# Kernel optimization log

Hardware: AMD Instinct MI355X
Metric: run time of the kernel (lower is better)

## Reference

```python
import jax, jax.numpy as jnp
import numpy as np

P_LEN, Q_LEN, BATCH, D, H = 300, 50, 32, 256, 256


def _make_params(key):
    ks = jax.random.split(key, 6)
    s = lambda k, shape, fan: jax.random.normal(k, shape, jnp.float32) * (1.0 / np.sqrt(fan))
    return dict(
        Wq=s(ks[0], (2, H, D), D), bq=jnp.zeros((2, H), jnp.float32),
        Wp=s(ks[1], (2, H, D), D), bp=jnp.zeros((2, H), jnp.float32),
        Wr=s(ks[2], (2, H, H), H), br=jnp.zeros((2, H), jnp.float32),
        Wg=s(ks[3], (2, H), H), bg=jnp.zeros((2,), jnp.float32),
        ln_g=jnp.ones((2, 2 * D), jnp.float32), ln_b=jnp.zeros((2, 2 * D), jnp.float32),
        W_ih=s(ks[4], (2, 4 * H, 2 * D), 2 * D), W_hh=s(ks[5], (2, 4 * H, H), H),
        b_ih=jnp.zeros((2, 4 * H), jnp.float32), b_hh=jnp.zeros((2, 4 * H), jnp.float32),
    )


def setup_inputs() -> dict:
    key = jax.random.key(0)
    k1, k2, k3, k4, kp = jax.random.split(key, 5)
    content_vec = jax.random.normal(k1, (P_LEN, BATCH, D), jnp.float32)
    question_vec = jax.random.normal(k2, (Q_LEN, BATCH, D), jnp.float32)
    p_len = jax.random.randint(k3, (BATCH,), P_LEN // 2, P_LEN + 1)
    q_len = jax.random.randint(k4, (BATCH,), Q_LEN // 2, Q_LEN + 1)
    content_mask = (jnp.arange(P_LEN)[None, :] < p_len[:, None]).astype(jnp.int32)
    question_mask = (jnp.arange(Q_LEN)[None, :] < q_len[:, None]).astype(jnp.int32)
    inp = dict(content_vec=content_vec, content_mask=content_mask,
               question_vec=question_vec, question_mask=question_mask)
    inp.update(_make_params(kp))
    return inp


def _masked_flip(v, mask):
    # v: (P, B, D); mask: (B, P). Reverses the valid prefix of each sequence,
    # leaving padding positions in place (standard Match-LSTM masked_flip).
    P = v.shape[0]
    lengths = mask.sum(axis=1)  # (B,)
    t = jnp.arange(P)[:, None]  # (P, 1)
    idx = jnp.where(t < lengths[None, :], lengths[None, :] - 1 - t, t)  # (P, B)
    idx = jnp.broadcast_to(idx[:, :, None], v.shape)
    return jnp.take_along_axis(v, idx, axis=0)


def _uni_match(cv, qv, qmask, Wq, bq, Wp, bp, Wr, br, Wg, bg, ln_g, ln_b, W_ih, W_hh, b_ih, b_hh):
    # cv: (P, B, D), qv: (Q, B, D), qmask: (B, Q)
    B = cv.shape[1]
    Hh = Wr.shape[0]
    wh = jnp.einsum('qbd,hd->qbh', qv, Wq) + bq      # (Q, B, H), precomputed once
    hp_all = jnp.einsum('pbd,hd->pbh', cv, Wp) + bp  # (P, B, H), precomputed
    pad = (qmask == 0)                               # (B, Q)

    def step(carry, xs):
        h, c = carry
        cv_t, hp_t = xs
        hr = h @ Wr.T + br                                    # (B, H)
        g = jnp.tanh(wh + hp_t[None] + hr[None])              # (Q, B, H)
        alpha = (jnp.einsum('qbh,h->qb', g, Wg) + bg).T       # (B, Q)
        alpha = jax.nn.softmax(jnp.where(pad, -jnp.inf, alpha), axis=1)
        h_alpha = jnp.einsum('bq,qbd->bd', alpha, qv)         # (B, D)
        z = jnp.concatenate([cv_t, h_alpha], axis=1)          # (B, 2D)
        mu = jnp.mean(z, axis=-1, keepdims=True)
        var = jnp.mean((z - mu) ** 2, axis=-1, keepdims=True)
        z = (z - mu) * jax.lax.rsqrt(var + 1e-5) * ln_g + ln_b
        gates = z @ W_ih.T + b_ih + h @ W_hh.T + b_hh         # (B, 4H)
        i_, f_, g_, o_ = jnp.split(gates, 4, axis=1)          # torch LSTMCell order i,f,g,o
        c_n = jax.nn.sigmoid(f_) * c + jax.nn.sigmoid(i_) * jnp.tanh(g_)
        h_n = jax.nn.sigmoid(o_) * jnp.tanh(c_n)
        return (h_n, c_n), h_n

    h0 = jnp.zeros((B, Hh), cv.dtype)
    _, hs = jax.lax.scan(step, (h0, h0), (cv, hp_all))
    return hs  # (P, B, H)


def reference(content_vec, content_mask, question_vec, question_mask,
              Wq, bq, Wp, bp, Wr, br, Wg, bg, ln_g, ln_b, W_ih, W_hh, b_ih, b_hh):
    # Dropout with p=0 (inference) is identity.
    args = lambda i: (Wq[i], bq[i], Wp[i], bp[i], Wr[i], br[i], Wg[i], bg[i],
                      ln_g[i], ln_b[i], W_ih[i], W_hh[i], b_ih[i], b_hh[i])
    right = _uni_match(content_vec, question_vec, question_mask, *args(0))
    cv_flip = _masked_flip(content_vec, content_mask)
    left = _uni_match(cv_flip, question_vec, question_mask, *args(1))
    left = _masked_flip(left, content_mask)
    res = jnp.concatenate([right, left], axis=2)            # (P, B, 2H)
    return content_mask.T[:, :, None].astype(res.dtype) * res
```

## Files before the change

kernel.cpp:

```cpp
#include <hip/hip_runtime.h>
#include <hip/hip_fp16.h>

typedef unsigned int u32;
typedef unsigned long long u64;
typedef _Float16 half2_t __attribute__((ext_vector_type(2)));
typedef _Float16 f16x8 __attribute__((ext_vector_type(8)));
typedef float f32x16 __attribute__((ext_vector_type(16)));

static constexpr int PL = 300;
static constexpr int QL = 50;
static constexpr int B  = 32;
static constexpr int D  = 256;
static constexpr int H  = 256;

__device__ __forceinline__ float fdot2(u32 w, u32 x, float acc) {
    return __builtin_amdgcn_fdot2(__builtin_bit_cast(half2_t, w),
                                  __builtin_bit_cast(half2_t, x), acc, false);
}
__device__ __forceinline__ u32 packh2(float a, float b) {
    half2_t h2; h2[0] = (_Float16)a; h2[1] = (_Float16)b;
    return __builtin_bit_cast(u32, h2);
}
__device__ __forceinline__ f32x16 mfma16(uint4 a, uint4 b, f32x16 c) {
    return __builtin_amdgcn_mfma_f32_32x32x16_f16(
        __builtin_bit_cast(f16x8, a), __builtin_bit_cast(f16x8, b), c, 0, 0, 0);
}
__device__ __forceinline__ u32 a_ld32(const u32* p) {
    return __hip_atomic_load(p, __ATOMIC_RELAXED, __HIP_MEMORY_SCOPE_AGENT);
}
__device__ __forceinline__ u64 a_ld64(const u64* p) {
    return __hip_atomic_load(p, __ATOMIC_RELAXED, __HIP_MEMORY_SCOPE_AGENT);
}
__device__ __forceinline__ void a_st32(u32* p, u32 v) {
    __hip_atomic_store(p, v, __ATOMIC_RELAXED, __HIP_MEMORY_SCOPE_AGENT);
}
__device__ __forceinline__ void a_st64(u64* p, u64 v) {
    __hip_atomic_store(p, v, __ATOMIC_RELAXED, __HIP_MEMORY_SCOPE_AGENT);
}

__global__ __launch_bounds__(256) void pack_wt2(const float* __restrict__ Whh,
                                                const float* __restrict__ Wr,
                                                u32* __restrict__ dst) {
    int id = blockIdx.x * 256 + threadIdx.x;
    int u  = id & 127;
    int rw = (id >> 7) % 40;
    int j  = ((id >> 7) / 40) % 32;
    int dd = (id >> 7) / 1280;
    float a, c;
    if (rw < 32) {
        int R = (rw >> 3) * 256 + 8 * j + (rw & 7);
        a = Whh[((size_t)dd * 1024 + R) * 256 + 2 * u];
        c = Whh[((size_t)dd * 1024 + R) * 256 + 2 * u + 1];
    } else {
        int wrr = 8 * j + (rw - 32);
        a = Wr[((size_t)dd * 256 + wrr) * 256 + 2 * u];
        c = Wr[((size_t)dd * 256 + wrr) * 256 + 2 * u + 1];
    }
    dst[id] = packh2(a, c);
}

__global__ __launch_bounds__(256) void prep_proj(const float* __restrict__ X,
                                                 const float* __restrict__ W,
                                                 const float* __restrict__ Bv,
                                                 __half* __restrict__ out,
                                                 int T, int nt) {
    int id = blockIdx.x;
    int tb = id % nt; id /= nt;
    int b  = id % B;  id /= B;
    int g  = id;
    int t0 = tb * 8;
    int nr = T - t0; if (nr > 8) nr = 8;
    __shared__ __align__(16) float xs[8][256];
    int tid = threadIdx.x;
    for (int r = 0; r < nr; r++) xs[r][tid] = X[((t0 + r) * B + b) * D + tid];
    __syncthreads();
    const float4* wrow = (const float4*)&W[(g * H + tid) * D];
    float bb = Bv[g * H + tid];
    float acc[8];
#pragma unroll
    for (int r = 0; r < 8; r++) acc[r] = bb;
    for (int d4 = 0; d4 < D / 4; d4++) {
        float4 w = wrow[d4];
#pragma unroll
        for (int r = 0; r < 8; r++) {
            float4 x = *(const float4*)&xs[r][d4 * 4];
            acc[r] = fmaf(w.x, x.x, fmaf(w.y, x.y, fmaf(w.z, x.z, fmaf(w.w, x.w, acc[r]))));
        }
    }
    for (int r = 0; r < nr; r++)
        out[((g * B + b) * T + t0 + r) * H + tid] = __float2half(acc[r]);
}

__global__ __launch_bounds__(256) void p1_prep(const float* __restrict__ cv,
                                               const float* __restrict__ Wih,
                                               const float* __restrict__ lng,
                                               __half* __restrict__ P1) {
    int id = blockIdx.x;
    int tb = id % 38; id /= 38;
    int b  = id % 32; id /= 32;
    int dd = id;
    int t0 = tb * 8;
    int nr = PL - t0; if (nr > 8) nr = 8;
    __shared__ __align__(16) float xs[8][256];
    int tid = threadIdx.x;
    float g = lng[dd * 512 + tid];
    for (int r = 0; r < nr; r++)
        xs[r][tid] = cv[((size_t)(t0 + r) * B + b) * D + tid] * g;
    __syncthreads();
    for (int gc = 0; gc < 4; gc++) {
        int R = gc * 256 + tid;
        const float4* wrow = (const float4*)&Wih[((size_t)dd * 1024 + R) * 512];
        float acc[8] = {};
        for (int d4 = 0; d4 < 64; d4++) {
            float4 w = wrow[d4];
#pragma unroll
            for (int r = 0; r < 8; r++) {
                float4 x = *(const float4*)&xs[r][d4 * 4];
                acc[r] = fmaf(w.x, x.x, fmaf(w.y, x.y, fmaf(w.z, x.z, fmaf(w.w, x.w, acc[r]))));
            }
        }
        for (int r = 0; r < nr; r++)
            P1[((size_t)(dd * 32 + b) * PL + t0 + r) * 1024 + R] = __float2half(acc[r]);
    }
}

__global__ __launch_bounds__(256) void vp_prep(const float* __restrict__ qv,
                                               const float* __restrict__ Wih,
                                               const float* __restrict__ lng,
                                               __half* __restrict__ VP) {
    int blk = blockIdx.x;
    int dd = blk >> 8, b = (blk >> 3) & 31, rc = blk & 7;
    __shared__ __align__(16) u32 qg[50 * 128];
    __shared__ __align__(16) u32 wch[128 * 128];
    int tid = threadIdx.x;
    for (int v = tid; v < 6400; v += 256) {
        int q = v >> 7, i = v & 127;
        float a = qv[((size_t)q * 32 + b) * 256 + 2 * i]     * lng[dd * 512 + 256 + 2 * i];
        float c = qv[((size_t)q * 32 + b) * 256 + 2 * i + 1] * lng[dd * 512 + 256 + 2 * i + 1];
        qg[v] = packh2(a, c);
    }
    for (int v = tid; v < 16384; v += 256) {
        int rl = v >> 7, i = v & 127;
        int r = rc * 128 + rl;
        float a = Wih[((size_t)dd * 1024 + r) * 512 + 256 + 2 * i];
        float c = Wih[((size_t)dd * 1024 + r) * 512 + 256 + 2 * i + 1];
        wch[v] = packh2(a, c);
    }
    __syncthreads();
    for (int p = tid; p < 128 * 56; p += 256) {
        int rl = p / 56, q = p % 56;
        int r = rc * 128 + rl;
        float acc = 0.f;
        if (q < 50) {
            const u32* qr = qg + q * 128;
            const u32* wr = wch + rl * 128;
#pragma unroll 8
            for (int i = 0; i < 128; i++) acc = fdot2(wr[i], qr[i], acc);
        }
        VP[((size_t)(dd * 32 + b) * 1024 + r) * 56 + q] = __float2half(acc);
    }
}

__global__ __launch_bounds__(256) void gram_prep(const float* __restrict__ qv,
                                                 float* __restrict__ G,
                                                 float* __restrict__ qs) {
    int b = blockIdx.x;
    __shared__ float qvs[50 * 256];
    int tid = threadIdx.x;
    for (int v = tid; v < 12800; v += 256) {
        int q = v >> 8, k = v & 255;
        qvs[v] = qv[((size_t)q * 32 + b) * 256 + k];
    }
    __syncthreads();
    for (int p = tid; p < 2500; p += 256) {
        int q = p / 50, q2 = p % 50;
        float acc = 0.f;
        for (int k = 0; k < 256; k++) acc = fmaf(qvs[q * 256 + k], qvs[q2 * 256 + k], acc);
        G[((size_t)b * 50 + q) * 50 + q2] = acc;
    }
    if (tid < 52) {
        float s = 0.f;
        if (tid < 50) for (int k = 0; k < 256; k++) s += qvs[tid * 256 + k];
        qs[b * 52 + tid] = s;
    }
}

__global__ __launch_bounds__(256) void cvstats_prep(const float* __restrict__ cv,
                                                    float* __restrict__ st) {
    int blk = blockIdx.x;
    int t = blk >> 5, b = blk & 31;
    int tid = threadIdx.x;
    float v = cv[((size_t)t * 32 + b) * 256 + tid];
    float s = v, s2 = v * v;
#pragma unroll
    for (int m = 32; m; m >>= 1) { s += __shfl_xor(s, m, 64); s2 += __shfl_xor(s2, m, 64); }
    __shared__ float red[8];
    if ((tid & 63) == 0) { red[(tid >> 6) * 2] = s; red[(tid >> 6) * 2 + 1] = s2; }
    __syncthreads();
    if (tid == 0) {
        float S = red[0] + red[2] + red[4] + red[6];
        float S2 = red[1] + red[3] + red[5] + red[7];
        st[((size_t)b * 300 + t) * 2] = S;
        st[((size_t)b * 300 + t) * 2 + 1] = S2;
    }
}

__global__ __launch_bounds__(256) void c1c2_prep(const float* __restrict__ Wih,
                                                 const float* __restrict__ lng,
                                                 const float* __restrict__ lnb,
                                                 const float* __restrict__ bih,
                                                 const float* __restrict__ bhh,
                                                 float* __restrict__ C12) {
    int id = blockIdx.x * 256 + threadIdx.x;
    int dd = id >> 10, R = id & 1023;
    float s1 = 0.f, s2 = 0.f;
    const float* wr = &Wih[((size_t)dd * 1024 + R) * 512];
    for (int k = 0; k < 512; k++) {
        float w = wr[k];
        s1 = fmaf(w, lng[dd * 512 + k], s1);
        s2 = fmaf(w, lnb[dd * 512 + k], s2);
    }
    C12[(size_t)id * 2] = s1;
    C12[(size_t)id * 2 + 1] = s2 + bih[dd * 1024 + R] + bhh[dd * 1024 + R];
}

__global__ __launch_bounds__(256, 1) void scan10(
    const int*   __restrict__ cmask,
    const int*   __restrict__ qmask,
    const float* __restrict__ Wgv,
    const float* __restrict__ bgv,
    const float* __restrict__ brp,
    const u32*   __restrict__ Wtp,
    const __half* __restrict__ whp,
    const __half* __restrict__ hpp,
    const __half* __restrict__ P1,
    const __half* __restrict__ VP,
    const float* __restrict__ C12,
    const float* __restrict__ G,
    const float* __restrict__ qsr,
    const float* __restrict__ cvst,
    u64* __restrict__ HX,
    u32* __restrict__ B2X,
    u32* __restrict__ B3X,
    float* __restrict__ out)
{
    int blk = blockIdx.x;
    int dd = blk >> 5, j = blk & 31;
    int tid = threadIdx.x;
    int lane = tid & 63, wave = tid >> 6;
    int rr = lane & 31, kh = lane >> 5, sw = rr & 7;

    __shared__ __align__(16) u32 sh_wt[40 * 128];
    __shared__ __align__(16) u32 sh_x[32 * 128];
    __shared__ __align__(16) u32 sh_wh[6400];
    __shared__ float sh_G[50 * 50];
    __shared__ float sh_red[4 * 32 * 33];
    __shared__ float sh_red3[4 * 32 * 8];
    __shared__ float sh_a[256];
    __shared__ float sh_af[64];
    __shared__ __align__(16) u32 sh_al2[28];
    __shared__ float sh_alpha[64];
    __shared__ float sh_qb[64];
    __shared__ float sh_qs[52];
    __shared__ float sh_r2[4];
    __shared__ float sh_cs[2];
    __shared__ int   sh_len[32];

    for (int v = tid; v < 40 * 128; v += 256) {
        int rl = v >> 7, u = v & 127;
        int c4 = u >> 2, w = u & 3;
        sh_wt[rl * 128 + (((c4 ^ (rl & 7)) << 2) | w)] =
            Wtp[((size_t)(dd * 32 + j) * 40 + rl) * 128 + u];
    }
    {
        const u32* whsrc = (const u32*)(whp + (size_t)(dd * 32 + j) * QL * H);
        for (int i = tid; i < 6400; i += 256) sh_wh[i] = whsrc[i];
    }
    for (int v = tid; v < 2500; v += 256) sh_G[v] = G[(size_t)j * 2500 + v];
    if (tid < 52) sh_qs[tid] = qsr[j * 52 + tid];
    if (tid < 64) sh_qb[tid] = (tid < QL) ? (qmask[j * QL + tid] ? 0.f : -1e30f) : -1e30f;
    if (tid < 32) sh_len[tid] = 0;
    __syncthreads();
    {
        int b = tid & 31, part = tid >> 5;
        int t0 = part * 38, t1 = t0 + 38 > PL ? PL : t0 + 38;
        int s = 0;
        for (int tt = t0; tt < t1; tt++) s += cmask[b * PL + tt];
        atomicAdd(&sh_len[b], s);
    }
    __syncthreads();

    float wgr[4];
#pragma unroll
    for (int i = 0; i < 4; i++) wgr[i] = Wgv[dd * H + lane + 64 * i];
    float bgs = bgv[dd];
    float brv = brp[dd * H + tid];
    float C1r[4], C2r[4];
#pragma unroll
    for (int k = 0; k < 4; k++) {
        C1r[k] = C12[((size_t)dd * 1024 + k * 256 + tid) * 2];
        C2r[k] = C12[((size_t)dd * 1024 + k * 256 + tid) * 2 + 1];
    }
    int len_j = sh_len[j];
    float c_reg = 0.f;

    for (int t = len_j; t < PL; t++)
        out[((size_t)t * B + j) * 512 + dd * 256 + tid] = 0.f;

    if (tid < 128) a_st64(HX + (size_t)(dd * 32 + j) * 128 + tid, ((u64)1 << 32));

    const __half* hpb = hpp + (size_t)(dd * 32 + j) * PL * H;
    const u32* VPu = (const u32*)VP;
    const u32* xrow  = sh_x + rr * 128;
    const u32* wrow  = sh_wt + rr * 128;
    const u32* wrow2 = sh_wt + (8 + rr) * 128;

    for (int t = 0; t < PL; t++) {
        u32 want = (u32)(t + 1);
        u32 want9 = want & 511;
        int tsj = dd ? (t < len_j ? len_j - 1 - t : t) : t;
        __syncthreads();

        float p1v[4];
#pragma unroll
        for (int k = 0; k < 4; k++)
            p1v[k] = __half2float(P1[((size_t)(dd * 32 + j) * PL + tsj) * 1024 + k * 256 + tid]);
        float hpv = __half2float(hpb[(size_t)tsj * H + tid]);
        if (tid == 0) {
            sh_cs[0] = cvst[((size_t)j * 300 + tsj) * 2];
            sh_cs[1] = cvst[((size_t)j * 300 + tsj) * 2 + 1];
        }

        {
            const u64* base = HX + (size_t)dd * 32 * 128;
            u64 v[16];
            for (;;) {
                bool ok = true;
#pragma unroll
                for (int m = 0; m < 16; m++) v[m] = a_ld64(base + m * 256 + tid);
#pragma unroll
                for (int m = 0; m < 16; m++) ok &= ((u32)(v[m] >> 32) == want);
                if (ok) break;
                __builtin_amdgcn_s_sleep(2);
            }
#pragma unroll
            for (int m = 0; m < 16; m++) {
                int w = m * 256 + tid;
                int b = w >> 7, c2 = w & 127;
                sh_x[b * 128 + (((c2 >> 2) ^ (b & 7)) << 2) + (c2 & 3)] = (u32)v[m];
            }
        }
        __syncthreads();

        {
            f32x16 acc1 = {}, acc2 = {};
#pragma unroll
            for (int kk = 0; kk < 4; kk++) {
                int c4 = wave * 8 + 2 * kk + kh;
                int pc4 = (c4 ^ sw) << 2;
                uint4 au = *(const uint4*)(xrow + pc4);
                uint4 b1 = *(const uint4*)(wrow + pc4);
                uint4 b2 = *(const uint4*)(wrow2 + pc4);
                acc1 = mfma16(au, b1, acc1);
                acc2 = mfma16(au, b2, acc2);
            }
#pragma unroll
            for (int q = 0; q < 16; q++) {
                int b = (q & 3) + 8 * (q >> 2) + 4 * kh;
                sh_red[(wave * 32 + b) * 33 + rr] = acc1[q];
            }
            if (rr >= 24) {
#pragma unroll
                for (int q = 0; q < 16; q++) {
                    int b = (q & 3) + 8 * (q >> 2) + 4 * kh;
                    sh_red3[(wave * 32 + b) * 8 + (rr - 24)] = acc2[q];
                }
            }
        }
        __syncthreads();

        {
            int bb = tid >> 3, rq = (tid & 7) * 4;
            u32* dst = B2X + (size_t)(dd * 32 + bb) * 1024 + j * 32 + rq;
#pragma unroll
            for (int i = 0; i < 4; i++) {
                float f = sh_red[(0 * 32 + bb) * 33 + rq + i] + sh_red[(1 * 32 + bb) * 33 + rq + i]
                        + sh_red[(2 * 32 + bb) * 33 + rq + i] + sh_red[(3 * 32 + bb) * 33 + rq + i];
                a_st32(dst + i, (__builtin_bit_cast(u32, f) & ~511u) | want9);
            }
            int rw = tid & 7;
            float b3 = sh_red3[bb * 8 + rw] + sh_red3[(32 + bb) * 8 + rw]
                     + sh_red3[(64 + bb) * 8 + rw] + sh_red3[(96 + bb) * 8 + rw];
            a_st32(B3X + (size_t)(dd * 32 + bb) * 256 + 8 * j + rw,
                   (__builtin_bit_cast(u32, b3) & ~511u) | want9);
        }

        uint4 vp[28];
#pragma unroll
        for (int k = 0; k < 4; k++) {
            const uint4* vr = (const uint4*)(VPu + ((size_t)(dd * 32 + j) * 1024 + k * 256 + tid) * 28);
#pragma unroll
            for (int i = 0; i < 7; i++) vp[k * 7 + i] = vr[i];
        }

        float bg2[4], hrv;
        {
            const u32* b2b = B2X + (size_t)(dd * 32 + j) * 1024 + (tid >> 3) * 32 + (tid & 7);
            const u32* b3b = B3X + (size_t)(dd * 32 + j) * 256 + tid;
            u32 v0, v1, v2, v3, v4;
            for (;;) {
                v0 = a_ld32(b2b);
                v1 = a_ld32(b2b + 8);
                v2 = a_ld32(b2b + 16);
                v3 = a_ld32(b2b + 24);
                v4 = a_ld32(b3b);
                bool ok = ((v0 & 511) == want9) & ((v1 & 511) == want9)
                        & ((v2 & 511) == want9) & ((v3 & 511) == want9)
                        & ((v4 & 511) == want9);
                if (ok) break;
                __builtin_amdgcn_s_sleep(2);
            }
            bg2[0] = __builtin_bit_cast(float, v0 & ~511u);
            bg2[1] = __builtin_bit_cast(float, v1 & ~511u);
            bg2[2] = __builtin_bit_cast(float, v2 & ~511u);
            bg2[3] = __builtin_bit_cast(float, v3 & ~511u);
            hrv    = __builtin_bit_cast(float, v4 & ~511u);
            sh_a[tid] = hrv + brv + hpv;
        }
        __syncthreads();

        {
            float av[4];
#pragma unroll
            for (int i = 0; i < 4; i++) av[i] = sh_a[lane + 64 * i];
            const __half* wh16 = (const __half*)sh_wh;
            for (int q = wave; q < QL; q += 4) {
                float a = 0.f;
#pragma unroll
                for (int i = 0; i < 4; i++) {
                    float xx = (float)wh16[q * 256 + lane + 64 * i] + av[i];
                    float e = __expf(2.f * xx);
                    a = fmaf(wgr[i], (e - 1.f) / (e + 1.f), a);
                }
#pragma unroll
                for (int m = 32; m; m >>= 1) a += __shfl_xor(a, m, 64);
                if (lane == 0) sh_alpha[q] = a + bgs + sh_qb[q];
            }
        }
        __syncthreads();

        if (wave == 0) {
            float v = (lane < QL) ? sh_alpha[lane] : -1e30f;
            float m = v;
#pragma unroll
            for (int s = 32; s; s >>= 1) m = fmaxf(m, __shfl_xor(m, s, 64));
            float e = (lane < QL) ? __expf(v - m) : 0.f;
            float sum = e;
#pragma unroll
            for (int s = 32; s; s >>= 1) sum += __shfl_xor(sum, s, 64);
            float al = (lane < QL) ? e / sum : 0.f;
            sh_af[lane] = al;
            float alo = __shfl_xor(al, 1, 64);
            if (!(lane & 1) && lane < 56) sh_al2[lane >> 1] = packh2(al, alo);
        }
        __syncthreads();

        if (wave == 0) {
            float gd = 0.f;
            if (lane < QL) {
                const float* Grow = sh_G + lane * 50;
                float aq = sh_af[lane];
                for (int q2 = 0; q2 < QL; q2++) gd = fmaf(Grow[q2], sh_af[q2], gd);
                gd *= aq;
            }
#pragma unroll
            for (int m = 32; m; m >>= 1) gd += __shfl_xor(gd, m, 64);
            if (lane == 0) sh_r2[0] = gd;
        } else if (wave == 1) {
            float s = (lane < QL) ? sh_af[lane] * sh_qs[lane] : 0.f;
#pragma unroll
            for (int m = 32; m; m >>= 1) s += __shfl_xor(s, m, 64);
            if (lane == 0) sh_r2[1] = s;
        }
        __syncthreads();

        float aVP[4];
#pragma unroll
        for (int k = 0; k < 4; k++) {
            float acc = 0.f;
#pragma unroll
            for (int i = 0; i < 7; i++) {
                acc = fdot2(vp[k * 7 + i].x, sh_al2[i * 4 + 0], acc);
                acc = fdot2(vp[k * 7 + i].y, sh_al2[i * 4 + 1], acc);
                acc = fdot2(vp[k * 7 + i].z, sh_al2[i * 4 + 2], acc);
                acc = fdot2(vp[k * 7 + i].w, sh_al2[i * 4 + 3], acc);
            }
            aVP[k] = acc;
        }

        float hv;
        {
            float mu = (sh_cs[0] + sh_r2[1]) * (1.f / 512.f);
            float E2 = (sh_cs[1] + sh_r2[0]) * (1.f / 512.f);
            float rs = rsqrtf(E2 - mu * mu + 1e-5f);
            float gk[4];
#pragma unroll
            for (int k = 0; k < 4; k++)
                gk[k] = rs * (p1v[k] + aVP[k]) - rs * mu * C1r[k] + C2r[k] + bg2[k];
            float si = 1.f / (1.f + __expf(-gk[0]));
            float sf = 1.f / (1.f + __expf(-gk[1]));
            float so = 1.f / (1.f + __expf(-gk[3]));
            float eg = __expf(2.f * gk[2]); float tg = (eg - 1.f) / (eg + 1.f);
            float c = sf * c_reg + si * tg;
            float ec = __expf(2.f * c); float tc = (ec - 1.f) / (ec + 1.f);
            hv = so * tc;
            c_reg = c;
            float ho = __shfl_xor(hv, 1, 64);
            if (!(tid & 1))
                a_st64(HX + (size_t)(dd * 32 + j) * 128 + (tid >> 1),
                       (((u64)(t + 2)) << 32) | (u64)packh2(hv, ho));
        }

        if (t < len_j)
            out[((size_t)tsj * B + j) * 512 + dd * 256 + tid] = hv;
    }
}

extern "C" void kernel_launch(void* const* d_in, const int* in_sizes, int n_in,
                              void* d_out, int out_size, void* d_ws, size_t ws_size,
                              hipStream_t stream) {
    const float* cv    = (const float*)d_in[0];
    const int*   cmask = (const int*)  d_in[1];
    const float* qv    = (const float*)d_in[2];
    const int*   qmask = (const int*)  d_in[3];
    const float* Wq    = (const float*)d_in[4];
    const float* bq    = (const float*)d_in[5];
    const float* Wp    = (const float*)d_in[6];
    const float* bp    = (const float*)d_in[7];
    const float* Wr    = (const float*)d_in[8];
    const float* br    = (const float*)d_in[9];
    const float* Wg    = (const float*)d_in[10];
    const float* bg    = (const float*)d_in[11];
    const float* ln_g  = (const float*)d_in[12];
    const float* ln_b  = (const float*)d_in[13];
    const float* Wih   = (const float*)d_in[14];
    const float* Whh   = (const float*)d_in[15];
    const float* b_ih  = (const float*)d_in[16];
    const float* b_hh  = (const float*)d_in[17];
    float* out = (float*)d_out;

    uint8_t* ws = (uint8_t*)d_ws;
    u32*    Wtp = (u32*)ws;      ws += (size_t)2 * 32 * 40 * 128 * 4;
    __half* VP  = (__half*)ws;   ws += (size_t)2 * 32 * 1024 * 56 * 2;
    __half* whp = (__half*)ws;   ws += (size_t)2 * 32 * 50 * 256 * 2;
    __half* hpp = (__half*)ws;   ws += (size_t)2 * 32 * 300 * 256 * 2;
    __half* P1  = (__half*)ws;   ws += (size_t)2 * 32 * 300 * 1024 * 2;
    float*  C12 = (float*)ws;    ws += (size_t)2 * 1024 * 2 * 4;
    float*  G   = (float*)ws;    ws += (size_t)32 * 50 * 50 * 4;
    float*  qs  = (float*)ws;    ws += (size_t)32 * 52 * 4;
    float*  cvs = (float*)ws;    ws += (size_t)32 * 300 * 2 * 4;
    u64* HX  = (u64*)ws;         ws += (size_t)2 * 32 * 128 * 8;
    u32* B2X = (u32*)ws;         ws += (size_t)2 * 32 * 1024 * 4;
    u32* B3X = (u32*)ws;         ws += (size_t)2 * 32 * 256 * 4;

    hipMemsetAsync(HX, 0, (size_t)2 * 32 * 128 * 8 + (size_t)2 * 32 * 1024 * 4
                          + (size_t)2 * 32 * 256 * 4, stream);
    hipLaunchKernelGGL(pack_wt2, dim3(1280), dim3(256), 0, stream, Whh, Wr, Wtp);
    hipLaunchKernelGGL(prep_proj, dim3(2 * 32 * 7), dim3(256), 0, stream,
                       qv, Wq, bq, whp, QL, 7);
    hipLaunchKernelGGL(prep_proj, dim3(2 * 32 * 38), dim3(256), 0, stream,
                       cv, Wp, bp, hpp, PL, 38);
    hipLaunchKernelGGL(p1_prep, dim3(2 * 32 * 38), dim3(256), 0, stream,
                       cv, Wih, ln_g, P1);
    hipLaunchKernelGGL(vp_prep, dim3(512), dim3(256), 0, stream, qv, Wih, ln_g, VP);
    hipLaunchKernelGGL(gram_prep, dim3(32), dim3(256), 0, stream, qv, G, qs);
    hipLaunchKernelGGL(cvstats_prep, dim3(9600), dim3(256), 0, stream, cv, cvs);
    hipLaunchKernelGGL(c1c2_prep, dim3(8), dim3(256), 0, stream,
                       Wih, ln_g, ln_b, b_ih, b_hh, C12);
    hipLaunchKernelGGL(scan10, dim3(64), dim3(256), 0, stream,
                       cmask, qmask, Wg, bg, br, Wtp, whp, hpp, P1, VP, C12, G, qs, cvs,
                       HX, B2X, B3X, out);
}
```

Baseline: 4.026 ms.

## Compute Wr·h locally per block instead of distributed MFMA with cross-block exchange

Each of the 64 persistent blocks now computes the full Wr·h_{t-1} term for its own batch element using fdot2 over its local copy of the previous hidden state in LDS, reading packed fp16 Wr rows from global memory. This removes the B3X cross-block exchange and its spin-wait, and drops the second MFMA and shared reduction. The B2X wait is moved later, after the attention work, so it overlaps with compute. The cost is 128 KB of Wr reads per block per step, served from L2, plus 256 dot products of length 256 per thread each step.

```diff
diff --git a/kernel.cpp b/kernel.cpp
--- a/kernel.cpp
+++ b/kernel.cpp
@@ -38,25 +38,27 @@
     __hip_atomic_store(p, v, __ATOMIC_RELAXED, __HIP_MEMORY_SCOPE_AGENT);
 }
 
-__global__ __launch_bounds__(256) void pack_wt2(const float* __restrict__ Whh,
-                                                const float* __restrict__ Wr,
+__global__ __launch_bounds__(256) void pack_wt3(const float* __restrict__ Whh,
                                                 u32* __restrict__ dst) {
     int id = blockIdx.x * 256 + threadIdx.x;
     int u  = id & 127;
-    int rw = (id >> 7) % 40;
-    int j  = ((id >> 7) / 40) % 32;
-    int dd = (id >> 7) / 1280;
-    float a, c;
-    if (rw < 32) {
-        int R = (rw >> 3) * 256 + 8 * j + (rw & 7);
-        a = Whh[((size_t)dd * 1024 + R) * 256 + 2 * u];
-        c = Whh[((size_t)dd * 1024 + R) * 256 + 2 * u + 1];
-    } else {
-        int wrr = 8 * j + (rw - 32);
-        a = Wr[((size_t)dd * 256 + wrr) * 256 + 2 * u];
-        c = Wr[((size_t)dd * 256 + wrr) * 256 + 2 * u + 1];
-    }
+    int rw = (id >> 7) % 32;
+    int j  = ((id >> 7) / 32) % 32;
+    int dd = (id >> 7) / 1024;
+    int R = (rw >> 3) * 256 + 8 * j + (rw & 7);
+    float a = Whh[((size_t)dd * 1024 + R) * 256 + 2 * u];
+    float c = Whh[((size_t)dd * 1024 + R) * 256 + 2 * u + 1];
     dst[id] = packh2(a, c);
+}
+
+__global__ __launch_bounds__(256) void pack_wr_rows(const float* __restrict__ W,
+                                                    u32* __restrict__ dst) {
+    int id = blockIdx.x * 256 + threadIdx.x;
+    int g = id / 32768;
+    int rem = id % 32768;
+    int r = rem / 128, u = rem % 128;
+    const float* s = &W[(g * 256 + r) * 256 + 2 * u];
+    dst[id] = packh2(s[0], s[1]);
 }
 
 __global__ __launch_bounds__(256) void prep_proj(const float* __restrict__ X,
@@ -224,13 +226,14 @@
     C12[(size_t)id * 2 + 1] = s2 + bih[dd * 1024 + R] + bhh[dd * 1024 + R];
 }
 
-__global__ __launch_bounds__(256, 1) void scan10(
+__global__ __launch_bounds__(256, 1) void scan11(
     const int*   __restrict__ cmask,
     const int*   __restrict__ qmask,
     const float* __restrict__ Wgv,
     const float* __restrict__ bgv,
     const float* __restrict__ brp,
     const u32*   __restrict__ Wtp,
+    const u32*   __restrict__ Wrp,
     const __half* __restrict__ whp,
     const __half* __restrict__ hpp,
     const __half* __restrict__ P1,
@@ -241,7 +244,6 @@
     const float* __restrict__ cvst,
     u64* __restrict__ HX,
     u32* __restrict__ B2X,
-    u32* __restrict__ B3X,
     float* __restrict__ out)
 {
     int blk = blockIdx.x;
@@ -250,12 +252,11 @@
     int lane = tid & 63, wave = tid >> 6;
     int rr = lane & 31, kh = lane >> 5, sw = rr & 7;
 
-    __shared__ __align__(16) u32 sh_wt[40 * 128];
+    __shared__ __align__(16) u32 sh_wt[32 * 128];
     __shared__ __align__(16) u32 sh_x[32 * 128];
     __shared__ __align__(16) u32 sh_wh[6400];
     __shared__ float sh_G[50 * 50];
     __shared__ float sh_red[4 * 32 * 33];
-    __shared__ float sh_red3[4 * 32 * 8];
     __shared__ float sh_a[256];
     __shared__ float sh_af[64];
     __shared__ __align__(16) u32 sh_al2[28];
@@ -265,12 +266,13 @@
     __shared__ float sh_r2[4];
     __shared__ float sh_cs[2];
     __shared__ int   sh_len[32];
-
-    for (int v = tid; v < 40 * 128; v += 256) {
+    __shared__ __align__(16) u32 sh_hj[128];
+
+    for (int v = tid; v < 32 * 128; v += 256) {
         int rl = v >> 7, u = v & 127;
         int c4 = u >> 2, w = u & 3;
         sh_wt[rl * 128 + (((c4 ^ (rl & 7)) << 2) | w)] =
-            Wtp[((size_t)(dd * 32 + j) * 40 + rl) * 128 + u];
+            Wtp[((size_t)(dd * 32 + j) * 32 + rl) * 128 + u];
     }
     {
         const u32* whsrc = (const u32*)(whp + (size_t)(dd * 32 + j) * QL * H);
@@ -279,6 +281,7 @@
     for (int v = tid; v < 2500; v += 256) sh_G[v] = G[(size_t)j * 2500 + v];
     if (tid < 52) sh_qs[tid] = qsr[j * 52 + tid];
     if (tid < 64) sh_qb[tid] = (tid < QL) ? (qmask[j * QL + tid] ? 0.f : -1e30f) : -1e30f;
+    if (tid < 128) sh_hj[tid] = 0;
     if (tid < 32) sh_len[tid] = 0;
     __syncthreads();
     {
@@ -311,9 +314,9 @@
 
     const __half* hpb = hpp + (size_t)(dd * 32 + j) * PL * H;
     const u32* VPu = (const u32*)VP;
-    const u32* xrow  = sh_x + rr * 128;
-    const u32* wrow  = sh_wt + rr * 128;
-    const u32* wrow2 = sh_wt + (8 + rr) * 128;
+    const uint4* wr4 = (const uint4*)(Wrp + ((size_t)dd * 256 + tid) * 128);
+    const u32* xrow = sh_x + rr * 128;
+    const u32* wrow = sh_wt + rr * 128;
 
     for (int t = 0; t < PL; t++) {
         u32 want = (u32)(t + 1);
@@ -332,6 +335,18 @@
         }
 
         {
+            float p0 = 0.f, p1 = 0.f, p2 = 0.f, p3 = 0.f;
+#pragma unroll 8
+            for (int kk = 0; kk < 32; kk++) {
+                uint4 w = wr4[kk];
+                uint4 hx = *(const uint4*)(sh_hj + kk * 4);
+                p0 = fdot2(w.x, hx.x, p0); p1 = fdot2(w.y, hx.y, p1);
+                p2 = fdot2(w.z, hx.z, p2); p3 = fdot2(w.w, hx.w, p3);
+            }
+            sh_a[tid] = (p0 + p1) + (p2 + p3) + brv + hpv;
+        }
+
+        {
             const u64* base = HX + (size_t)dd * 32 * 128;
             u64 v[16];
             for (;;) {
@@ -353,28 +368,19 @@
         __syncthreads();
 
         {
-            f32x16 acc1 = {}, acc2 = {};
+            f32x16 acc1 = {};
 #pragma unroll
             for (int kk = 0; kk < 4; kk++) {
                 int c4 = wave * 8 + 2 * kk + kh;
                 int pc4 = (c4 ^ sw) << 2;
                 uint4 au = *(const uint4*)(xrow + pc4);
                 uint4 b1 = *(const uint4*)(wrow + pc4);
-                uint4 b2 = *(const uint4*)(wrow2 + pc4);
                 acc1 = mfma16(au, b1, acc1);
-                acc2 = mfma16(au, b2, acc2);
             }
 #pragma unroll
             for (int q = 0; q < 16; q++) {
                 int b = (q & 3) + 8 * (q >> 2) + 4 * kh;
                 sh_red[(wave * 32 + b) * 33 + rr] = acc1[q];
-            }
-            if (rr >= 24) {
-#pragma unroll
-                for (int q = 0; q < 16; q++) {
-                    int b = (q & 3) + 8 * (q >> 2) + 4 * kh;
-                    sh_red3[(wave * 32 + b) * 8 + (rr - 24)] = acc2[q];
-                }
             }
         }
         __syncthreads();
@@ -388,11 +394,6 @@
                         + sh_red[(2 * 32 + bb) * 33 + rq + i] + sh_red[(3 * 32 + bb) * 33 + rq + i];
                 a_st32(dst + i, (__builtin_bit_cast(u32, f) & ~511u) | want9);
             }
-            int rw = tid & 7;
-            float b3 = sh_red3[bb * 8 + rw] + sh_red3[(32 + bb) * 8 + rw]
-                     + sh_red3[(64 + bb) * 8 + rw] + sh_red3[(96 + bb) * 8 + rw];
-            a_st32(B3X + (size_t)(dd * 32 + bb) * 256 + 8 * j + rw,
-                   (__builtin_bit_cast(u32, b3) & ~511u) | want9);
         }
 
         uint4 vp[28];
@@ -402,32 +403,6 @@
 #pragma unroll
             for (int i = 0; i < 7; i++) vp[k * 7 + i] = vr[i];
         }
-
-        float bg2[4], hrv;
-        {
-            const u32* b2b = B2X + (size_t)(dd * 32 + j) * 1024 + (tid >> 3) * 32 + (tid & 7);
-            const u32* b3b = B3X + (size_t)(dd * 32 + j) * 256 + tid;
-            u32 v0, v1, v2, v3, v4;
-            for (;;) {
-                v0 = a_ld32(b2b);
-                v1 = a_ld32(b2b + 8);
-                v2 = a_ld32(b2b + 16);
-                v3 = a_ld32(b2b + 24);
-                v4 = a_ld32(b3b);
-                bool ok = ((v0 & 511) == want9) & ((v1 & 511) == want9)
-                        & ((v2 & 511) == want9) & ((v3 & 511) == want9)
-                        & ((v4 & 511) == want9);
-                if (ok) break;
-                __builtin_amdgcn_s_sleep(2);
-            }
-            bg2[0] = __builtin_bit_cast(float, v0 & ~511u);
-            bg2[1] = __builtin_bit_cast(float, v1 & ~511u);
-            bg2[2] = __builtin_bit_cast(float, v2 & ~511u);
-            bg2[3] = __builtin_bit_cast(float, v3 & ~511u);
-            hrv    = __builtin_bit_cast(float, v4 & ~511u);
-            sh_a[tid] = hrv + brv + hpv;
-        }
-        __syncthreads();
 
         {
             float av[4];
@@ -496,6 +471,26 @@
                 acc = fdot2(vp[k * 7 + i].w, sh_al2[i * 4 + 3], acc);
             }
             aVP[k] = acc;
+        }
+
+        float bg2[4];
+        {
+            const u32* b2b = B2X + (size_t)(dd * 32 + j) * 1024 + (tid >> 3) * 32 + (tid & 7);
+            u32 v0, v1, v2, v3;
+            for (;;) {
+                v0 = a_ld32(b2b);
+                v1 = a_ld32(b2b + 8);
+                v2 = a_ld32(b2b + 16);
+                v3 = a_ld32(b2b + 24);
+                bool ok = ((v0 & 511) == want9) & ((v1 & 511) == want9)
+                        & ((v2 & 511) == want9) & ((v3 & 511) == want9);
+                if (ok) break;
+                __builtin_amdgcn_s_sleep(2);
+            }
+            bg2[0] = __builtin_bit_cast(float, v0 & ~511u);
+            bg2[1] = __builtin_bit_cast(float, v1 & ~511u);
+            bg2[2] = __builtin_bit_cast(float, v2 & ~511u);
+            bg2[3] = __builtin_bit_cast(float, v3 & ~511u);
         }
 
         float hv;
@@ -516,9 +511,12 @@
             hv = so * tc;
             c_reg = c;
             float ho = __shfl_xor(hv, 1, 64);
-            if (!(tid & 1))
+            if (!(tid & 1)) {
+                u32 pk = packh2(hv, ho);
+                sh_hj[tid >> 1] = pk;
                 a_st64(HX + (size_t)(dd * 32 + j) * 128 + (tid >> 1),
-                       (((u64)(t + 2)) << 32) | (u64)packh2(hv, ho));
+                       (((u64)(t + 2)) << 32) | (u64)pk);
+            }
         }
 
         if (t < len_j)
@@ -550,7 +548,8 @@
     float* out = (float*)d_out;
 
     uint8_t* ws = (uint8_t*)d_ws;
-    u32*    Wtp = (u32*)ws;      ws += (size_t)2 * 32 * 40 * 128 * 4;
+    u32*    Wtp = (u32*)ws;      ws += (size_t)2 * 32 * 32 * 128 * 4;
+    u32*    Wrp = (u32*)ws;      ws += (size_t)2 * 256 * 128 * 4;
     __half* VP  = (__half*)ws;   ws += (size_t)2 * 32 * 1024 * 56 * 2;
     __half* whp = (__half*)ws;   ws += (size_t)2 * 32 * 50 * 256 * 2;
     __half* hpp = (__half*)ws;   ws += (size_t)2 * 32 * 300 * 256 * 2;
@@ -561,11 +560,10 @@
     float*  cvs = (float*)ws;    ws += (size_t)32 * 300 * 2 * 4;
     u64* HX  = (u64*)ws;         ws += (size_t)2 * 32 * 128 * 8;
     u32* B2X = (u32*)ws;         ws += (size_t)2 * 32 * 1024 * 4;
-    u32* B3X = (u32*)ws;         ws += (size_t)2 * 32 * 256 * 4;
-
-    hipMemsetAsync(HX, 0, (size_t)2 * 32 * 128 * 8 + (size_t)2 * 32 * 1024 * 4
-                          + (size_t)2 * 32 * 256 * 4, stream);
-    hipLaunchKernelGGL(pack_wt2, dim3(1280), dim3(256), 0, stream, Whh, Wr, Wtp);
+
+    hipMemsetAsync(HX, 0, (size_t)2 * 32 * 128 * 8 + (size_t)2 * 32 * 1024 * 4, stream);
+    hipLaunchKernelGGL(pack_wt3, dim3(1024), dim3(256), 0, stream, Whh, Wtp);
+    hipLaunchKernelGGL(pack_wr_rows, dim3(256), dim3(256), 0, stream, Wr, Wrp);
     hipLaunchKernelGGL(prep_proj, dim3(2 * 32 * 7), dim3(256), 0, stream,
                        qv, Wq, bq, whp, QL, 7);
     hipLaunchKernelGGL(prep_proj, dim3(2 * 32 * 38), dim3(256), 0, stream,
@@ -577,7 +575,7 @@
     hipLaunchKernelGGL(cvstats_prep, dim3(9600), dim3(256), 0, stream, cv, cvs);
     hipLaunchKernelGGL(c1c2_prep, dim3(8), dim3(256), 0, stream,
                        Wih, ln_g, ln_b, b_ih, b_hh, C12);
-    hipLaunchKernelGGL(scan10, dim3(64), dim3(256), 0, stream,
-                       cmask, qmask, Wg, bg, br, Wtp, whp, hpp, P1, VP, C12, G, qs, cvs,
-                       HX, B2X, B3X, out);
-}
+    hipLaunchKernelGGL(scan11, dim3(64), dim3(256), 0, stream,
+                       cmask, qmask, Wg, bg, br, Wtp, Wrp, whp, hpp, P1, VP, C12, G, qs, cvs,
+                       HX, B2X, out);
+}
```

New measurement: 4.649 ms. 1.15x slower.
